# Kernel optimization log

Hardware: AMD Instinct MI355X
Metric: run time of the kernel (lower is better)

## Reference

```python
import jax, jax.numpy as jnp
import numpy as np

ALPHA = 0.2  # leaky_relu negative slope
NEG = -1e12


def setup_inputs() -> dict:
    key = jax.random.key(0)
    k1, k2, k3, k4 = jax.random.split(key, 4)
    N, FIN, FOUT = 8192, 128, 64
    inp = jax.random.normal(k1, (N, FIN), dtype=jnp.float32)
    adj = jax.random.randint(k2, (N, N), 0, 2, dtype=jnp.int32)
    W = jax.random.normal(k3, (FIN, FOUT), dtype=jnp.float32) * 0.1
    a = jax.random.normal(k4, (2 * FOUT, 1), dtype=jnp.float32) * 0.1
    return {"inp": inp, "adj": adj, "W": W, "a": a}


def reference(inp, adj, W, a):
    # h: [N, F]
    h = inp @ W
    F = h.shape[1]
    # additive decomposition of a^T [h_i ; h_j] = (h @ a1)_i + (h @ a2)_j
    a1 = a[:F, 0]
    a2 = a[F:, 0]
    s1 = h @ a1  # [N]
    s2 = h @ a2  # [N]
    e = jax.nn.leaky_relu(s1[:, None] + s2[None, :], negative_slope=ALPHA)  # [N, N]
    att = jnp.where(adj > 0, e, jnp.float32(NEG))
    att = jax.nn.softmax(att, axis=1)
    # dropout is identity in eval mode (training=False)
    h_prime = att @ h  # [N, F]
    return jax.nn.elu(h_prime)  # concat=True
```

## Files before the change

kernel.cpp:

```cpp
#include <hip/hip_runtime.h>

typedef __attribute__((ext_vector_type(8))) short short8;
typedef __attribute__((ext_vector_type(4))) float f32x4;
typedef __attribute__((ext_vector_type(4))) int   i32x4;
typedef unsigned long long u64;

#define NN 8192
#define FIN 128
#define FOUT 64
#define LRELU_ALPHA 0.2f
#define SHIFT_B 10.0f

__device__ __forceinline__ unsigned short f2bf(float x) {
    unsigned u = __float_as_uint(x);
    unsigned r = (u + 0x7FFFu + ((u >> 16) & 1u)) >> 16;
    return (unsigned short)r;
}

__device__ __forceinline__ unsigned vcol_of(unsigned i) {
    return (i & ~63u) | ((i & 3u) << 4) | ((i & 63u) >> 2);
}

__global__ __launch_bounds__(256) void gat_prep(
    const float* __restrict__ inp, const float* __restrict__ W,
    const float* __restrict__ a,
    unsigned short* __restrict__ htp, float* __restrict__ s1,
    float* __restrict__ e1v, float* __restrict__ e2v)
{
    __shared__ float Wl[FIN * FOUT];
    __shared__ float il[4 * FIN];
    const int tid = threadIdx.x;
    const int i0 = blockIdx.x * 4;

    #pragma unroll
    for (int k = 0; k < (FIN * FOUT) / 256; ++k)
        Wl[tid + 256 * k] = W[tid + 256 * k];
    #pragma unroll
    for (int k = 0; k < (4 * FIN) / 256; ++k)
        il[tid + 256 * k] = inp[(size_t)i0 * FIN + tid + 256 * k];
    __syncthreads();

    const int r = tid >> 6;
    const int f = tid & 63;
    float acc = 0.f;
    #pragma unroll 8
    for (int k = 0; k < FIN; ++k)
        acc = fmaf(il[r * FIN + k], Wl[k * FOUT + f], acc);

    float v1 = acc * a[f];
    float v2 = acc * a[FOUT + f];
    #pragma unroll
    for (int off = 32; off; off >>= 1) {
        v1 += __shfl_xor(v1, off, 64);
        v2 += __shfl_xor(v2, off, 64);
    }
    const int i = i0 + r;
    const unsigned vc = vcol_of((unsigned)i);
    if (f == 0) {
        s1[i] = v1;
        e1v[vc] = __expf(v2);
        e2v[vc] = __expf(LRELU_ALPHA * v2);
    }
    const unsigned Tt = vc >> 6, ic = vc & 63u;
    const unsigned ss = ic >> 5, kk = (ic >> 3) & 3u, ee = ic & 7u;
    const unsigned fb = (unsigned)f >> 4, ll = (unsigned)f & 15u;
    htp[((Tt * 8u + ss * 4u + fb) << 9) + ((kk * 16u + ll) << 3) + ee] = f2bf(acc);
}

#define ADJ_ISSUE(P, tt) do {                                                 \
    const unsigned oa_ = vadj0 + (unsigned)(tt) * 256u;                       \
    asm volatile("global_load_dwordx4 %0, %1, %2"                             \
                 : "=v"(P##0) : "v"(oa_), "s"(adjb));                         \
    asm volatile("global_load_dwordx4 %0, %1, %2"                             \
                 : "=v"(P##1) : "v"(oa_ + 131072u), "s"(adjb));               \
    asm volatile("global_load_dwordx4 %0, %1, %2"                             \
                 : "=v"(P##2) : "v"(oa_ + 262144u), "s"(adjb));               \
    asm volatile("global_load_dwordx4 %0, %1, %2"                             \
                 : "=v"(P##3) : "v"(oa_ + 393216u), "s"(adjb));               \
} while (0)

#define HTP_ISSUE(P, tt) do {                                                 \
    const unsigned oh_  = vhtp0 + (unsigned)(tt) * 8192u;                     \
    const unsigned oh2_ = oh_ + 4096u;                                        \
    asm volatile("global_load_dwordx4 %0, %1, %2 offset:0"                    \
                 : "=v"(P##_h0) : "v"(oh_), "s"(htpb));                       \
    asm volatile("global_load_dwordx4 %0, %1, %2 offset:1024"                 \
                 : "=v"(P##_h1) : "v"(oh_), "s"(htpb));                       \
    asm volatile("global_load_dwordx4 %0, %1, %2 offset:2048"                 \
                 : "=v"(P##_h2) : "v"(oh_), "s"(htpb));                       \
    asm volatile("global_load_dwordx4 %0, %1, %2 offset:3072"                 \
                 : "=v"(P##_h3) : "v"(oh_), "s"(htpb));                       \
    asm volatile("global_load_dwordx4 %0, %1, %2 offset:0"                    \
                 : "=v"(P##_h4) : "v"(oh2_), "s"(htpb));                      \
    asm volatile("global_load_dwordx4 %0, %1, %2 offset:1024"                 \
                 : "=v"(P##_h5) : "v"(oh2_), "s"(htpb));                      \
    asm volatile("global_load_dwordx4 %0, %1, %2 offset:2048"                 \
                 : "=v"(P##_h6) : "v"(oh2_), "s"(htpb));                      \
    asm volatile("global_load_dwordx4 %0, %1, %2 offset:3072"                 \
                 : "=v"(P##_h7) : "v"(oh2_), "s"(htpb));                      \
} while (0)

#define BALLOT1(V, rr, MBL, MBH) do {                                         \
    const u64 b0_ = __ballot(V[0] > 0);                                       \
    const u64 b1_ = __ballot(V[1] > 0);                                       \
    const u64 b2_ = __ballot(V[2] > 0);                                       \
    const u64 b3_ = __ballot(V[3] > 0);                                       \
    const u64 sA_ = (kg & 2) ? b1_ : b0_;                                     \
    const u64 sB_ = (kg & 2) ? b3_ : b2_;                                     \
    const unsigned m0_ = (unsigned)(sA_ >> sh) & 0xffu;                       \
    const unsigned m1_ = (unsigned)(sB_ >> sh) & 0xffu;                       \
    MBL = (myr == (rr)) ? m0_ : MBL;                                          \
    MBH = (myr == (rr)) ? m1_ : MBH;                                          \
} while (0)

#define BALLOT4(P, MBL, MBH) do {                                             \
    BALLOT1(P##0, 0, MBL, MBH);                                               \
    BALLOT1(P##1, 1, MBL, MBH);                                               \
    BALLOT1(P##2, 2, MBL, MBH);                                               \
    BALLOT1(P##3, 3, MBL, MBH);                                               \
} while (0)

#define COMPUTE(B0_, B1_, B2_, B3_, MB, uu) do {                              \
    const int eo_ = (uu) * 32 + 8 * kg;                                       \
    const f32x4 E1a_ = *(const f32x4*)&e1l[eo_];                              \
    const f32x4 E1b_ = *(const f32x4*)&e1l[eo_ + 4];                          \
    const f32x4 E2a_ = *(const f32x4*)&e2l[eo_];                              \
    const f32x4 E2b_ = *(const f32x4*)&e2l[eo_ + 4];                          \
    float p_[8];                                                              \
    _Pragma("unroll")                                                         \
    for (int e = 0; e < 8; ++e) {                                             \
        const float e1_ = (e < 4) ? E1a_[e] : E1b_[e - 4];                    \
        const float e2_ = (e < 4) ? E2a_[e] : E2b_[e - 4];                    \
        const float pv_ = fmaxf(c1 * e1_, c2 * e2_);                          \
        p_[e] = (((MB) >> e) & 1u) ? pv_ : 0.f;                               \
        lsum += p_[e];                                                        \
    }                                                                         \
    union { short8 s8; unsigned u4[4]; } afu_;                                \
    _Pragma("unroll")                                                         \
    for (int q = 0; q < 4; ++q) {                                             \
        unsigned rr_;                                                         \
        asm("v_cvt_pk_bf16_f32 %0, %1, %2"                                    \
            : "=v"(rr_) : "v"(p_[2 * q]), "v"(p_[2 * q + 1]));                \
        afu_.u4[q] = rr_;                                                     \
    }                                                                         \
    acc0 = __builtin_amdgcn_mfma_f32_16x16x32_bf16(afu_.s8, B0_, acc0, 0,0,0);\
    acc1 = __builtin_amdgcn_mfma_f32_16x16x32_bf16(afu_.s8, B1_, acc1, 0,0,0);\
    acc2 = __builtin_amdgcn_mfma_f32_16x16x32_bf16(afu_.s8, B2_, acc2, 0,0,0);\
    acc3 = __builtin_amdgcn_mfma_f32_16x16x32_bf16(afu_.s8, B3_, acc3, 0,0,0);\
} while (0)

#define ITER(P, tt, W) do {                                                   \
    asm volatile("s_waitcnt vmcnt(" #W ")" ::: "memory");                     \
    __builtin_amdgcn_sched_barrier(0);                                        \
    unsigned mbl_ = 0, mbh_ = 0;                                              \
    BALLOT4(P, mbl_, mbh_);                                                   \
    if ((tt) + 2 < nt) ADJ_ISSUE(P, (tt) + 2);                                \
    COMPUTE(P##_h0, P##_h1, P##_h2, P##_h3, mbl_, 2 * (tt));                  \
    COMPUTE(P##_h4, P##_h5, P##_h6, P##_h7, mbh_, 2 * (tt) + 1);              \
    if ((tt) + 2 < nt) HTP_ISSUE(P, (tt) + 2);                                \
} while (0)

__global__ __launch_bounds__(256, 2) void gat_attn(
    const int* __restrict__ adj, const unsigned short* __restrict__ htp,
    const float* __restrict__ s1, const float* __restrict__ e1v,
    const float* __restrict__ e2v,
    float* __restrict__ pacc, float* __restrict__ pl, int jlen)
{
    __shared__ float e1l[2048];
    __shared__ float e2l[2048];

    const int w    = threadIdx.x >> 6;
    const int lane = threadIdx.x & 63;
    const int lo   = lane & 15;
    const int kg   = lane >> 4;
    const int i0   = blockIdx.x * 64;
    const int i    = i0 + w * 16 + lo;
    const int jstart = blockIdx.y * jlen;
    const int nt     = jlen >> 6;

    for (int x = threadIdx.x; x < (jlen >> 2); x += 256) {
        ((f32x4*)e1l)[x] = *(const f32x4*)(e1v + jstart + 4 * x);
        ((f32x4*)e2l)[x] = *(const f32x4*)(e2v + jstart + 4 * x);
    }
    __syncthreads();

    const float s1v = s1[i];
    const float mm  = s1v + SHIFT_B;
    const float Mi  = fmaxf(mm, LRELU_ALPHA * mm);
    const float c1  = __expf(s1v - Mi);
    const float c2  = __expf(LRELU_ALPHA * s1v - Mi);

    const int      myr = lo >> 2;
    const unsigned sh  = ((lo & 3) << 4) | ((kg & 1) << 3);

    const int* adjb = adj + (size_t)i0 * NN;
    const unsigned short* htpb = htp;
    const unsigned vadj0 = (unsigned)((((w * 16 + kg) * NN) + (lane & 15) * 4 + jstart) * 4);
    const unsigned vhtp0 = (unsigned)(((unsigned)(jstart >> 6) * 8192u) + lane * 16);

    f32x4 acc0 = {0.f,0.f,0.f,0.f}, acc1 = {0.f,0.f,0.f,0.f};
    f32x4 acc2 = {0.f,0.f,0.f,0.f}, acc3 = {0.f,0.f,0.f,0.f};
    float lsum = 0.f;

    i32x4 X0, X1, X2, X3, Y0, Y1, Y2, Y3;
    short8 X_h0, X_h1, X_h2, X_h3, X_h4, X_h5, X_h6, X_h7;
    short8 Y_h0, Y_h1, Y_h2, Y_h3, Y_h4, Y_h5, Y_h6, Y_h7;

    __builtin_amdgcn_sched_barrier(0);
    ADJ_ISSUE(X, 0); HTP_ISSUE(X, 0);
    ADJ_ISSUE(Y, 1); HTP_ISSUE(Y, 1);

    for (int k2 = 0; k2 < nt / 2 - 1; ++k2) {
        const int t0 = 2 * k2;
        ITER(X, t0, 12);
        ITER(Y, t0 + 1, 12);
    }
    ITER(X, nt - 2, 12);
    ITER(Y, nt - 1, 0);

    lsum += __shfl_xor(lsum, 16, 64);
    lsum += __shfl_xor(lsum, 32, 64);
    if (kg == 0)
        pl[(size_t)blockIdx.y * NN + i] = lsum;

    float* pa = pacc + ((size_t)blockIdx.y * NN + i0 + w * 16) * FOUT;
    #pragma unroll
    for (int reg = 0; reg < 4; ++reg) {
        const int orow = kg * 4 + reg;
        pa[(size_t)orow * FOUT + 0 * 16 + lo] = acc0[reg];
        pa[(size_t)orow * FOUT + 1 * 16 + lo] = acc1[reg];
        pa[(size_t)orow * FOUT + 2 * 16 + lo] = acc2[reg];
        pa[(size_t)orow * FOUT + 3 * 16 + lo] = acc3[reg];
    }
}

__global__ __launch_bounds__(256) void gat_reduce(
    const float* __restrict__ pacc, const float* __restrict__ pl,
    float* __restrict__ out, int JS)
{
    const int q = blockIdx.x * 256 + threadIdx.x;
    const int i = q >> 4;
    float l = 0.f;
    f32x4 v = {0.f, 0.f, 0.f, 0.f};
    for (int js = 0; js < JS; ++js) {
        l += pl[(size_t)js * NN + i];
        const f32x4 pv = *(const f32x4*)(pacc + (size_t)js * NN * FOUT + 4 * q);
        v[0] += pv[0]; v[1] += pv[1]; v[2] += pv[2]; v[3] += pv[3];
    }
    const float rl = 1.f / l;
    f32x4 o;
    #pragma unroll
    for (int e = 0; e < 4; ++e) {
        const float r = v[e] * rl;
        o[e] = r > 0.f ? r : expm1f(r);
    }
    *(f32x4*)(out + 4 * q) = o;
}

extern "C" void kernel_launch(void* const* d_in, const int* in_sizes, int n_in,
                              void* d_out, int out_size, void* d_ws, size_t ws_size,
                              hipStream_t stream)
{
    const float* inp = (const float*)d_in[0];
    const int*   adj = (const int*)d_in[1];
    const float* W   = (const float*)d_in[2];
    const float* a   = (const float*)d_in[3];
    float* out = (float*)d_out;

    char* ws = (char*)d_ws;
    unsigned short* htp = (unsigned short*)ws; ws += (size_t)FOUT * NN * 2;
    float* s1  = (float*)ws; ws += (size_t)NN * 4;
    float* e1v = (float*)ws; ws += (size_t)NN * 4;
    float* e2v = (float*)ws; ws += (size_t)NN * 4;

    const int JS = 8;
    const int jlen = NN / JS;

    float* pl   = (float*)ws; ws += (size_t)JS * NN * 4;
    float* pacc = (float*)ws;

    gat_prep  <<<NN / 4, 256, 0, stream>>>(inp, W, a, htp, s1, e1v, e2v);
    gat_attn  <<<dim3(NN / 64, JS), 256, 0, stream>>>(adj, htp, s1, e1v, e2v, pacc, pl, jlen);
    gat_reduce<<<(NN * FOUT) / 1024, 256, 0, stream>>>(pacc, pl, out, JS);
}
```

Before: 82.10 us.

## Pre-pack adjacency into bitmask kernel and drop ballot decoding in attention

Adds a separate gat_mask kernel that compresses the int32 adjacency matrix into 64-bit-per-tile bitmasks. gat_attn then stages each block's mask words in LDS instead of streaming adj and decoding it with ballots. The htp and e1/e2 layouts switch to natural column order to match the new mask bit order. This removes the adjacency loads and ballot work from the attention loop, at the cost of an extra kernel launch, an extra mask write and read, and losing the overlap between adjacency streaming and the attention math.

```diff
diff --git a/kernel.cpp b/kernel.cpp
--- a/kernel.cpp
+++ b/kernel.cpp
@@ -8,6 +8,7 @@
 #define NN 8192
 #define FIN 128
 #define FOUT 64
+#define NT (NN / 64)
 #define LRELU_ALPHA 0.2f
 #define SHIFT_B 10.0f
 
@@ -15,10 +16,6 @@
     unsigned u = __float_as_uint(x);
     unsigned r = (u + 0x7FFFu + ((u >> 16) & 1u)) >> 16;
     return (unsigned short)r;
-}
-
-__device__ __forceinline__ unsigned vcol_of(unsigned i) {
-    return (i & ~63u) | ((i & 3u) << 4) | ((i & 63u) >> 2);
 }
 
 __global__ __launch_bounds__(256) void gat_prep(
@@ -55,29 +52,37 @@
         v2 += __shfl_xor(v2, off, 64);
     }
     const int i = i0 + r;
-    const unsigned vc = vcol_of((unsigned)i);
     if (f == 0) {
         s1[i] = v1;
-        e1v[vc] = __expf(v2);
-        e2v[vc] = __expf(LRELU_ALPHA * v2);
-    }
-    const unsigned Tt = vc >> 6, ic = vc & 63u;
-    const unsigned ss = ic >> 5, kk = (ic >> 3) & 3u, ee = ic & 7u;
+        e1v[i] = __expf(v2);
+        e2v[i] = __expf(LRELU_ALPHA * v2);
+    }
+    const unsigned c = (unsigned)i;
+    const unsigned Tt = c >> 6, ss = (c >> 5) & 1u, kk = (c >> 3) & 3u, ee = c & 7u;
     const unsigned fb = (unsigned)f >> 4, ll = (unsigned)f & 15u;
     htp[((Tt * 8u + ss * 4u + fb) << 9) + ((kk * 16u + ll) << 3) + ee] = f2bf(acc);
 }
 
-#define ADJ_ISSUE(P, tt) do {                                                 \
-    const unsigned oa_ = vadj0 + (unsigned)(tt) * 256u;                       \
-    asm volatile("global_load_dwordx4 %0, %1, %2"                             \
-                 : "=v"(P##0) : "v"(oa_), "s"(adjb));                         \
-    asm volatile("global_load_dwordx4 %0, %1, %2"                             \
-                 : "=v"(P##1) : "v"(oa_ + 131072u), "s"(adjb));               \
-    asm volatile("global_load_dwordx4 %0, %1, %2"                             \
-                 : "=v"(P##2) : "v"(oa_ + 262144u), "s"(adjb));               \
-    asm volatile("global_load_dwordx4 %0, %1, %2"                             \
-                 : "=v"(P##3) : "v"(oa_ + 393216u), "s"(adjb));               \
-} while (0)
+__global__ __launch_bounds__(256) void gat_mask(const int* __restrict__ adj,
+                                                unsigned* __restrict__ mask)
+{
+    const int gid = blockIdx.x * 256 + threadIdx.x;
+    const int* p = adj + (size_t)gid * 32;
+
+    i32x4 v[8];
+    #pragma unroll
+    for (int q = 0; q < 8; ++q)
+        v[q] = *(const i32x4*)(p + q * 4);
+
+    unsigned m = 0;
+    #pragma unroll
+    for (int q = 0; q < 8; ++q) {
+        #pragma unroll
+        for (int e = 0; e < 4; ++e)
+            m |= (v[q][e] > 0 ? 1u : 0u) << (q * 4 + e);
+    }
+    mask[gid] = m;
+}
 
 #define HTP_ISSUE(P, tt) do {                                                 \
     const unsigned oh_  = vhtp0 + (unsigned)(tt) * 8192u;                     \
@@ -98,26 +103,6 @@
                  : "=v"(P##_h6) : "v"(oh2_), "s"(htpb));                      \
     asm volatile("global_load_dwordx4 %0, %1, %2 offset:3072"                 \
                  : "=v"(P##_h7) : "v"(oh2_), "s"(htpb));                      \
-} while (0)
-
-#define BALLOT1(V, rr, MBL, MBH) do {                                         \
-    const u64 b0_ = __ballot(V[0] > 0);                                       \
-    const u64 b1_ = __ballot(V[1] > 0);                                       \
-    const u64 b2_ = __ballot(V[2] > 0);                                       \
-    const u64 b3_ = __ballot(V[3] > 0);                                       \
-    const u64 sA_ = (kg & 2) ? b1_ : b0_;                                     \
-    const u64 sB_ = (kg & 2) ? b3_ : b2_;                                     \
-    const unsigned m0_ = (unsigned)(sA_ >> sh) & 0xffu;                       \
-    const unsigned m1_ = (unsigned)(sB_ >> sh) & 0xffu;                       \
-    MBL = (myr == (rr)) ? m0_ : MBL;                                          \
-    MBH = (myr == (rr)) ? m1_ : MBH;                                          \
-} while (0)
-
-#define BALLOT4(P, MBL, MBH) do {                                             \
-    BALLOT1(P##0, 0, MBL, MBH);                                               \
-    BALLOT1(P##1, 1, MBL, MBH);                                               \
-    BALLOT1(P##2, 2, MBL, MBH);                                               \
-    BALLOT1(P##3, 3, MBL, MBH);                                               \
 } while (0)
 
 #define COMPUTE(B0_, B1_, B2_, B3_, MB, uu) do {                              \
@@ -152,22 +137,23 @@
 #define ITER(P, tt, W) do {                                                   \
     asm volatile("s_waitcnt vmcnt(" #W ")" ::: "memory");                     \
     __builtin_amdgcn_sched_barrier(0);                                        \
-    unsigned mbl_ = 0, mbh_ = 0;                                              \
-    BALLOT4(P, mbl_, mbh_);                                                   \
-    if ((tt) + 2 < nt) ADJ_ISSUE(P, (tt) + 2);                                \
+    const u64 mw_ = ml[mlrow + (tt)];                                         \
+    const unsigned mbl_ = (unsigned)(mw_ >> (8 * kg)) & 0xffu;                \
+    const unsigned mbh_ = (unsigned)(mw_ >> (32 + 8 * kg)) & 0xffu;           \
     COMPUTE(P##_h0, P##_h1, P##_h2, P##_h3, mbl_, 2 * (tt));                  \
     COMPUTE(P##_h4, P##_h5, P##_h6, P##_h7, mbh_, 2 * (tt) + 1);              \
     if ((tt) + 2 < nt) HTP_ISSUE(P, (tt) + 2);                                \
 } while (0)
 
 __global__ __launch_bounds__(256, 2) void gat_attn(
-    const int* __restrict__ adj, const unsigned short* __restrict__ htp,
+    const u64* __restrict__ mask, const unsigned short* __restrict__ htp,
     const float* __restrict__ s1, const float* __restrict__ e1v,
     const float* __restrict__ e2v,
     float* __restrict__ pacc, float* __restrict__ pl, int jlen)
 {
-    __shared__ float e1l[2048];
-    __shared__ float e2l[2048];
+    __shared__ float e1l[1024];
+    __shared__ float e2l[1024];
+    __shared__ u64   ml[64 * 17];
 
     const int w    = threadIdx.x >> 6;
     const int lane = threadIdx.x & 63;
@@ -182,6 +168,13 @@
         ((f32x4*)e1l)[x] = *(const f32x4*)(e1v + jstart + 4 * x);
         ((f32x4*)e2l)[x] = *(const f32x4*)(e2v + jstart + 4 * x);
     }
+    {
+        const u64* mbase = mask + (size_t)i0 * NT + (jstart >> 6);
+        for (int x = threadIdx.x; x < 64 * 16; x += 256) {
+            const int r_ = x >> 4, t_ = x & 15;
+            ml[r_ * 17 + t_] = mbase[(size_t)r_ * NT + t_];
+        }
+    }
     __syncthreads();
 
     const float s1v = s1[i];
@@ -190,32 +183,27 @@
     const float c1  = __expf(s1v - Mi);
     const float c2  = __expf(LRELU_ALPHA * s1v - Mi);
 
-    const int      myr = lo >> 2;
-    const unsigned sh  = ((lo & 3) << 4) | ((kg & 1) << 3);
-
-    const int* adjb = adj + (size_t)i0 * NN;
+    const int mlrow = (w * 16 + lo) * 17;
     const unsigned short* htpb = htp;
-    const unsigned vadj0 = (unsigned)((((w * 16 + kg) * NN) + (lane & 15) * 4 + jstart) * 4);
     const unsigned vhtp0 = (unsigned)(((unsigned)(jstart >> 6) * 8192u) + lane * 16);
 
     f32x4 acc0 = {0.f,0.f,0.f,0.f}, acc1 = {0.f,0.f,0.f,0.f};
     f32x4 acc2 = {0.f,0.f,0.f,0.f}, acc3 = {0.f,0.f,0.f,0.f};
     float lsum = 0.f;
 
-    i32x4 X0, X1, X2, X3, Y0, Y1, Y2, Y3;
     short8 X_h0, X_h1, X_h2, X_h3, X_h4, X_h5, X_h6, X_h7;
     short8 Y_h0, Y_h1, Y_h2, Y_h3, Y_h4, Y_h5, Y_h6, Y_h7;
 
     __builtin_amdgcn_sched_barrier(0);
-    ADJ_ISSUE(X, 0); HTP_ISSUE(X, 0);
-    ADJ_ISSUE(Y, 1); HTP_ISSUE(Y, 1);
+    HTP_ISSUE(X, 0);
+    HTP_ISSUE(Y, 1);
 
     for (int k2 = 0; k2 < nt / 2 - 1; ++k2) {
         const int t0 = 2 * k2;
-        ITER(X, t0, 12);
-        ITER(Y, t0 + 1, 12);
-    }
-    ITER(X, nt - 2, 12);
+        ITER(X, t0, 8);
+        ITER(Y, t0 + 1, 8);
+    }
+    ITER(X, nt - 2, 8);
     ITER(Y, nt - 1, 0);
 
     lsum += __shfl_xor(lsum, 16, 64);
@@ -269,6 +257,7 @@
 
     char* ws = (char*)d_ws;
     unsigned short* htp = (unsigned short*)ws; ws += (size_t)FOUT * NN * 2;
+    u64* mask = (u64*)ws; ws += (size_t)NN * NT * 8;
     float* s1  = (float*)ws; ws += (size_t)NN * 4;
     float* e1v = (float*)ws; ws += (size_t)NN * 4;
     float* e2v = (float*)ws; ws += (size_t)NN * 4;
@@ -279,7 +268,8 @@
     float* pl   = (float*)ws; ws += (size_t)JS * NN * 4;
     float* pacc = (float*)ws;
 
+    gat_mask  <<<(NN * (NN / 32)) / 256, 256, 0, stream>>>(adj, (unsigned*)mask);
     gat_prep  <<<NN / 4, 256, 0, stream>>>(inp, W, a, htp, s1, e1v, e2v);
-    gat_attn  <<<dim3(NN / 64, JS), 256, 0, stream>>>(adj, htp, s1, e1v, e2v, pacc, pl, jlen);
+    gat_attn  <<<dim3(NN / 64, JS), 256, 0, stream>>>(mask, htp, s1, e1v, e2v, pacc, pl, jlen);
     gat_reduce<<<(NN * FOUT) / 1024, 256, 0, stream>>>(pacc, pl, out, JS);
 }
```

New measurement: 88.53 us. 1.08x slower.
